# Kernel tuning notes

Measured on AMD Instinct MI355X. Metric: run time of the kernel, lower is better.

The kernel has to match this reference:

```python
import jax, jax.numpy as jnp
import numpy as np

T = 64
LAMBDA_SCALE = 4
RECON = 512
U = 2 ** (LAMBDA_SCALE - 1)          # 8
YT = RECON // U                      # 64
P = YT * YT                          # 4096


def convert_Ht2Weights(Ht, u):
    # Ht: [T, recon, recon] -> per-low-res-pixel weights [P, T, u*u]
    t, r, _ = Ht.shape
    yt = r // u
    w = Ht.reshape(t, yt, u, yt, u)
    w = jnp.transpose(w, (1, 3, 0, 2, 4))        # [yt, yt, T, u, u]
    return w.reshape(yt * yt, t, u * u)


def setup_inputs() -> dict:
    key = jax.random.key(0)
    k1, k2, k3 = jax.random.split(key, 3)
    yt = jax.random.normal(k1, (64, T, YT, YT), dtype=jnp.float32)
    Ht = jax.random.normal(k2, (T, RECON, RECON), dtype=jnp.float32)
    biases = jax.random.normal(k3, (P, 1, U * U), dtype=jnp.float32)
    return {"yt": yt, "Ht": Ht, "biases": biases}


def reference(yt, Ht, biases):
    B = yt.shape[0]
    # [B, T, yt, yt] -> [P, B, T]
    y = yt.reshape(B, T, P).transpose(2, 0, 1)
    weights = convert_Ht2Weights(Ht, U)          # [P, T, u*u]
    # per-pixel batched GEMM + bias
    up = jnp.einsum('pbt,ptu->pbu', y, weights) + biases   # [P, B, u*u]
    # pixel-shuffle back to full resolution
    up = up.reshape(YT, YT, B, U, U)
    up = jnp.transpose(up, (2, 0, 3, 1, 4)).reshape(B, RECON, RECON)
    return up[:, None]                            # [B, 1, recon, recon] (seq_block = identity)
```

## Files before the change

### kernel.cpp

```cpp
#include <hip/hip_runtime.h>

typedef float f32x4 __attribute__((ext_vector_type(4)));
typedef short s16x8 __attribute__((ext_vector_type(8)));
typedef unsigned int u32;

__device__ __forceinline__ u32 f2bf(float x) {
    u32 u = __float_as_uint(x);
    return (u + 0x7FFFu + ((u >> 16) & 1u)) >> 16;
}
__device__ __forceinline__ u32 pk(float a, float b) {
    return f2bf(a) | (f2bf(b) << 16);
}
__device__ __forceinline__ int swz(int row, int t) {
    int g = ((row ^ (row >> 3)) & 7) << 3;
    return row * 64 + (t ^ g);
}
__device__ __forceinline__ int swzA(int row, int t) {
    return row * 64 + (t ^ ((row & 7) << 3));
}
__device__ __forceinline__ int bh(int rowid) {
    return (rowid ^ (rowid >> 4)) & 15;
}

#define A_PLANE 1032
#define A_SLOT  (8 * A_PLANE)
#define BOUNCE  (2 * A_SLOT)

__global__ __launch_bounds__(512, 4)
void upsample_mfma_kernel(const float* __restrict__ yt,
                          const float* __restrict__ Ht,
                          const float* __restrict__ biases,
                          float* __restrict__ out)
{
    __shared__ __align__(16) unsigned short S[32896];

    const int wg  = blockIdx.x;
    const int xcd = wg & 7;
    const int j   = wg >> 3;
    const int py  = xcd * 8 + (j & 7);
    const int pxo = j >> 3;
    const int px0 = pxo * 8;
    const int tid = (int)threadIdx.x;

    const int pxh = tid & 1;
    const int ab  = (tid >> 1) & 15;
    const int atq = tid >> 5;
    const float* a_base = yt + (size_t)ab * 262144 + (size_t)atq * 4 * 4096
                        + py * 64 + px0 + pxh * 4;

    f32x4 v[4];
    #pragma unroll
    for (int k = 0; k < 4; ++k)
        v[k] = *(const f32x4*)(a_base + (size_t)k * 4096);

    {
        const int c4 = tid & 15, uy = (tid >> 4) & 7, tq = tid >> 7;
        const float* wb = Ht + (size_t)(py * 8 + uy) * 512 + px0 * 8 + c4 * 4;
        #pragma unroll
        for (int ph = 0; ph < 2; ++ph) {
            const int t0 = ph * 32 + tq * 8;
            f32x4 w8[8];
            #pragma unroll
            for (int k = 0; k < 8; ++k)
                w8[k] = *(const f32x4*)(wb + (size_t)(t0 + k) * 262144);
            #pragma unroll
            for (int cc = 0; cc < 4; ++cc) {
                const int c = c4 * 4 + cc, pxl = c >> 3, uu = uy * 8 + (c & 7);
                uint4 g;
                g.x = pk(w8[0][cc], w8[1][cc]);
                g.y = pk(w8[2][cc], w8[3][cc]);
                g.z = pk(w8[4][cc], w8[5][cc]);
                g.w = pk(w8[6][cc], w8[7][cc]);
                *(uint4*)&S[pxl * 4096 + swz(uu, t0)] = g;
            }
        }
    }
    __syncthreads();

    const int wv = tid >> 6, l = tid & 63, r = l & 15, q = l >> 4;
    s16x8 wf[4][2];
    #pragma unroll
    for (int nb = 0; nb < 4; ++nb)
        #pragma unroll
        for (int ks = 0; ks < 2; ++ks)
            wf[nb][ks] = *(const s16x8*)&S[wv * 4096 + swz(nb * 16 + r, ks * 32 + q * 8)];
    const int px = px0 + wv, p = py * 64 + px;
    float bv[4];
    #pragma unroll
    for (int nb = 0; nb < 4; ++nb)
        bv[nb] = biases[(size_t)p * 64 + nb * 16 + r];
    __syncthreads();

    auto writeA = [&](int slot) {
        #pragma unroll
        for (int pp = 0; pp < 4; ++pp) {
            const int pxl = pxh * 4 + pp;
            *(uint2*)&S[slot * A_SLOT + pxl * A_PLANE + swzA(ab, atq * 4)] =
                make_uint2(pk(v[0][pp], v[1][pp]), pk(v[2][pp], v[3][pp]));
        }
    };
    auto issueA = [&](int chunk) {
        const float* ap = a_base + (size_t)chunk * 16 * 262144;
        #pragma unroll
        for (int k = 0; k < 4; ++k)
            v[k] = *(const f32x4*)(ap + (size_t)k * 4096);
    };

    writeA(0);
    issueA(1);
    __syncthreads();

    float* Sf = (float*)&S[BOUNCE];

    #pragma unroll
    for (int i = 0; i < 4; ++i) {
        f32x4 acc[4];
        #pragma unroll
        for (int nb = 0; nb < 4; ++nb)
            acc[nb] = (f32x4){bv[nb], bv[nb], bv[nb], bv[nb]};
        #pragma unroll
        for (int ks = 0; ks < 2; ++ks) {
            s16x8 af = *(const s16x8*)&S[(i & 1) * A_SLOT + wv * A_PLANE
                                         + swzA(r, ks * 32 + q * 8)];
            #pragma unroll
            for (int nb = 0; nb < 4; ++nb)
                acc[nb] = __builtin_amdgcn_mfma_f32_16x16x32_bf16(
                    af, wf[nb][ks], acc[nb], 0, 0, 0);
        }

        if (i < 3) {
            writeA((i + 1) & 1);
            if (i < 2) issueA(i + 2);
        }

        #pragma unroll
        for (int nb = 0; nb < 4; ++nb) {
            const int uy  = nb * 2 + (r >> 3);
            const int c4l = wv * 2 + ((r & 7) >> 2);
            const int e   = r & 3;
            #pragma unroll
            for (int ii = 0; ii < 4; ++ii) {
                const int bl    = q * 4 + ii;
                const int rowid = bl * 8 + uy;
                Sf[rowid * 64 + ((c4l ^ bh(rowid)) << 2) + e] = acc[nb][ii];
            }
        }
        __syncthreads();

        #pragma unroll
        for (int jj = 0; jj < 4; ++jj) {
            const int slot = jj * 512 + tid;
            const int bl = slot >> 7, rem = slot & 127;
            const int uy = rem >> 4, c4 = rem & 15;
            const int rowid = bl * 8 + uy;
            f32x4 vv = *(const f32x4*)&Sf[rowid * 64 + ((c4 ^ bh(rowid)) << 2)];
            *(f32x4*)&out[((size_t)(i * 16 + bl) * 512 + py * 8 + uy) * 512
                          + px0 * 8 + c4 * 4] = vv;
        }
        __syncthreads();
    }
}

extern "C" void kernel_launch(void* const* d_in, const int* in_sizes, int n_in,
                              void* d_out, int out_size, void* d_ws, size_t ws_size,
                              hipStream_t stream) {
    const float* yt     = (const float*)d_in[0];
    const float* Ht     = (const float*)d_in[1];
    const float* biases = (const float*)d_in[2];
    float* out          = (float*)d_out;
    upsample_mfma_kernel<<<dim3(512), dim3(512), 0, stream>>>(yt, Ht, biases, out);
}
```

Measured before the change: 36.75 us.

## Shrink LDS footprint with batch-8 chunks and double-buffered output bounce

The weight staging is split into two half-K phases over a smaller LDS region, and the batch chunk per iteration drops from 16 to 8 with eight iterations instead of four. The output bounce buffer is double-buffered so the trailing barrier per iteration is removed. Total shared memory falls and launch bounds rise to allow more resident workgroups. The cost is more MFMA-underutilized iterations (half the lanes idle on output writes) and an extra barrier during weight staging.

Result: slower. 83.06 us (+126.0%).

```diff
diff --git a/kernel.cpp b/kernel.cpp
--- a/kernel.cpp
+++ b/kernel.cpp
@@ -11,153 +11,149 @@
 __device__ __forceinline__ u32 pk(float a, float b) {
     return f2bf(a) | (f2bf(b) << 16);
 }
-__device__ __forceinline__ int swz(int row, int t) {
-    int g = ((row ^ (row >> 3)) & 7) << 3;
-    return row * 64 + (t ^ g);
-}
-__device__ __forceinline__ int swzA(int row, int t) {
-    return row * 64 + (t ^ ((row & 7) << 3));
-}
 __device__ __forceinline__ int bh(int rowid) {
     return (rowid ^ (rowid >> 4)) & 15;
 }
+__device__ __forceinline__ int g2(int uu) {
+    return (uu ^ (uu >> 2)) & 3;
+}
 
-#define A_PLANE 1032
-#define A_SLOT  (8 * A_PLANE)
-#define BOUNCE  (2 * A_SLOT)
+#define A_PLANE 520
+#define A_SLOT  4160
+#define SF_BASE 8320
 
-__global__ __launch_bounds__(512, 4)
+__global__ __launch_bounds__(512, 6)
 void upsample_mfma_kernel(const float* __restrict__ yt,
                           const float* __restrict__ Ht,
                           const float* __restrict__ biases,
                           float* __restrict__ out)
 {
-    __shared__ __align__(16) unsigned short S[32896];
+    __shared__ __align__(16) unsigned short S[24704];
 
     const int wg  = blockIdx.x;
-    const int xcd = wg & 7;
-    const int j   = wg >> 3;
-    const int py  = xcd * 8 + (j & 7);
-    const int pxo = j >> 3;
+    const int xcd = wg & 7, jj0 = wg >> 3;
+    const int py  = xcd * 8 + (jj0 & 7);
+    const int pxo = jj0 >> 3;
     const int px0 = pxo * 8;
     const int tid = (int)threadIdx.x;
 
     const int pxh = tid & 1;
-    const int ab  = (tid >> 1) & 15;
-    const int atq = tid >> 5;
-    const float* a_base = yt + (size_t)ab * 262144 + (size_t)atq * 4 * 4096
+    const int ab  = (tid >> 1) & 7;
+    const int atq = tid >> 4;
+    const float* a_base = yt + (size_t)ab * 262144 + (size_t)(atq * 2) * 4096
                         + py * 64 + px0 + pxh * 4;
 
-    f32x4 v[4];
+    f32x4 v0 = *(const f32x4*)(a_base);
+    f32x4 v1 = *(const f32x4*)(a_base + 4096);
+
+    const int c4 = tid & 15, w_uy = (tid >> 4) & 7, tq = tid >> 7;
+    const float* wb = Ht + (size_t)(py * 8 + w_uy) * 512 + px0 * 8 + c4 * 4;
+
+    const int wv = tid >> 6, l = tid & 63, r = l & 15, q = l >> 4;
+
+    s16x8 wf[4][2];
     #pragma unroll
-    for (int k = 0; k < 4; ++k)
-        v[k] = *(const f32x4*)(a_base + (size_t)k * 4096);
-
-    {
-        const int c4 = tid & 15, uy = (tid >> 4) & 7, tq = tid >> 7;
-        const float* wb = Ht + (size_t)(py * 8 + uy) * 512 + px0 * 8 + c4 * 4;
+    for (int h = 0; h < 2; ++h) {
+        if (h) __syncthreads();
+        f32x4 w8[8];
         #pragma unroll
-        for (int ph = 0; ph < 2; ++ph) {
-            const int t0 = ph * 32 + tq * 8;
-            f32x4 w8[8];
-            #pragma unroll
-            for (int k = 0; k < 8; ++k)
-                w8[k] = *(const f32x4*)(wb + (size_t)(t0 + k) * 262144);
-            #pragma unroll
-            for (int cc = 0; cc < 4; ++cc) {
-                const int c = c4 * 4 + cc, pxl = c >> 3, uu = uy * 8 + (c & 7);
-                uint4 g;
-                g.x = pk(w8[0][cc], w8[1][cc]);
-                g.y = pk(w8[2][cc], w8[3][cc]);
-                g.z = pk(w8[4][cc], w8[5][cc]);
-                g.w = pk(w8[6][cc], w8[7][cc]);
-                *(uint4*)&S[pxl * 4096 + swz(uu, t0)] = g;
-            }
+        for (int k = 0; k < 8; ++k)
+            w8[k] = *(const f32x4*)(wb + (size_t)(h * 32 + tq * 8 + k) * 262144);
+        #pragma unroll
+        for (int cc = 0; cc < 4; ++cc) {
+            const int c = c4 * 4 + cc, pxl = c >> 3, uu = w_uy * 8 + (c & 7);
+            uint4 g;
+            g.x = pk(w8[0][cc], w8[1][cc]);
+            g.y = pk(w8[2][cc], w8[3][cc]);
+            g.z = pk(w8[4][cc], w8[5][cc]);
+            g.w = pk(w8[6][cc], w8[7][cc]);
+            *(uint4*)&S[pxl * 2048 + uu * 32 + ((tq ^ g2(uu) ^ pxl) & 3) * 8] = g;
+        }
+        __syncthreads();
+        #pragma unroll
+        for (int nb = 0; nb < 4; ++nb) {
+            const int uu = nb * 16 + r;
+            wf[nb][h] = *(const s16x8*)&S[wv * 2048 + uu * 32
+                                          + ((q ^ g2(uu) ^ wv) & 3) * 8];
         }
     }
-    __syncthreads();
 
-    const int wv = tid >> 6, l = tid & 63, r = l & 15, q = l >> 4;
-    s16x8 wf[4][2];
+    const int p = py * 64 + px0 + wv;
+    float bv4[4];
     #pragma unroll
     for (int nb = 0; nb < 4; ++nb)
-        #pragma unroll
-        for (int ks = 0; ks < 2; ++ks)
-            wf[nb][ks] = *(const s16x8*)&S[wv * 4096 + swz(nb * 16 + r, ks * 32 + q * 8)];
-    const int px = px0 + wv, p = py * 64 + px;
-    float bv[4];
-    #pragma unroll
-    for (int nb = 0; nb < 4; ++nb)
-        bv[nb] = biases[(size_t)p * 64 + nb * 16 + r];
+        bv4[nb] = biases[(size_t)p * 64 + nb * 16 + r];
+
     __syncthreads();
 
     auto writeA = [&](int slot) {
+        const int col = (atq * 2) ^ (ab << 3);
         #pragma unroll
-        for (int pp = 0; pp < 4; ++pp) {
-            const int pxl = pxh * 4 + pp;
-            *(uint2*)&S[slot * A_SLOT + pxl * A_PLANE + swzA(ab, atq * 4)] =
-                make_uint2(pk(v[0][pp], v[1][pp]), pk(v[2][pp], v[3][pp]));
-        }
+        for (int pp = 0; pp < 4; ++pp)
+            *(u32*)&S[slot * A_SLOT + (pxh * 4 + pp) * A_PLANE + ab * 64 + col] =
+                pk(v0[pp], v1[pp]);
     };
     auto issueA = [&](int chunk) {
-        const float* ap = a_base + (size_t)chunk * 16 * 262144;
-        #pragma unroll
-        for (int k = 0; k < 4; ++k)
-            v[k] = *(const f32x4*)(ap + (size_t)k * 4096);
+        const float* ap = a_base + (size_t)chunk * 8 * 262144;
+        v0 = *(const f32x4*)(ap);
+        v1 = *(const f32x4*)(ap + 4096);
     };
 
     writeA(0);
     issueA(1);
     __syncthreads();
 
-    float* Sf = (float*)&S[BOUNCE];
+    float* Sf = (float*)&S[SF_BASE];
 
     #pragma unroll
-    for (int i = 0; i < 4; ++i) {
+    for (int i = 0; i < 8; ++i) {
         f32x4 acc[4];
         #pragma unroll
         for (int nb = 0; nb < 4; ++nb)
-            acc[nb] = (f32x4){bv[nb], bv[nb], bv[nb], bv[nb]};
+            acc[nb] = (f32x4){bv4[nb], bv4[nb], bv4[nb], bv4[nb]};
         #pragma unroll
         for (int ks = 0; ks < 2; ++ks) {
+            const int colA = (ks * 32 + q * 8) ^ ((r & 7) << 3);
             s16x8 af = *(const s16x8*)&S[(i & 1) * A_SLOT + wv * A_PLANE
-                                         + swzA(r, ks * 32 + q * 8)];
+                                         + (r & 7) * 64 + colA];
             #pragma unroll
             for (int nb = 0; nb < 4; ++nb)
                 acc[nb] = __builtin_amdgcn_mfma_f32_16x16x32_bf16(
                     af, wf[nb][ks], acc[nb], 0, 0, 0);
         }
 
-        if (i < 3) {
+        if (i < 7) {
             writeA((i + 1) & 1);
-            if (i < 2) issueA(i + 2);
+            if (i < 6) issueA(i + 2);
         }
 
-        #pragma unroll
-        for (int nb = 0; nb < 4; ++nb) {
-            const int uy  = nb * 2 + (r >> 3);
-            const int c4l = wv * 2 + ((r & 7) >> 2);
-            const int e   = r & 3;
+        if (q < 2) {
             #pragma unroll
-            for (int ii = 0; ii < 4; ++ii) {
-                const int bl    = q * 4 + ii;
-                const int rowid = bl * 8 + uy;
-                Sf[rowid * 64 + ((c4l ^ bh(rowid)) << 2) + e] = acc[nb][ii];
+            for (int nb = 0; nb < 4; ++nb) {
+                const int uyb = nb * 2 + (r >> 3);
+                const int c4l = wv * 2 + ((r & 7) >> 2);
+                const int e   = r & 3;
+                #pragma unroll
+                for (int ii = 0; ii < 4; ++ii) {
+                    const int rowid = (q * 4 + ii) * 8 + uyb;
+                    Sf[(i & 1) * 4096 + rowid * 64
+                       + ((c4l ^ bh(rowid)) << 2) + e] = acc[nb][ii];
+                }
             }
         }
         __syncthreads();
 
         #pragma unroll
-        for (int jj = 0; jj < 4; ++jj) {
+        for (int jj = 0; jj < 2; ++jj) {
             const int slot = jj * 512 + tid;
             const int bl = slot >> 7, rem = slot & 127;
-            const int uy = rem >> 4, c4 = rem & 15;
+            const int uy = rem >> 4, c4s = rem & 15;
             const int rowid = bl * 8 + uy;
-            f32x4 vv = *(const f32x4*)&Sf[rowid * 64 + ((c4 ^ bh(rowid)) << 2)];
-            *(f32x4*)&out[((size_t)(i * 16 + bl) * 512 + py * 8 + uy) * 512
-                          + px0 * 8 + c4 * 4] = vv;
+            f32x4 vv = *(const f32x4*)&Sf[(i & 1) * 4096 + rowid * 64
+                                          + ((c4s ^ bh(rowid)) << 2)];
+            *(f32x4*)&out[((size_t)(i * 8 + bl) * 512 + py * 8 + uy) * 512
+                          + px0 * 8 + c4s * 4] = vv;
         }
-        __syncthreads();
     }
 }
 
```
